# Performance work log

Measured on AMD Instinct MI355X. Metric: run time of the kernel, lower is better.

The kernel has to match this reference:

```python
import jax, jax.numpy as jnp
import numpy as np

VOCAB = 50257
EMBED = 256
UNITS = 1024   # dec_units == attention units == GRU units
ENC_D = 1024   # encoder feature dim
B = 64
T_ENC = 128


def setup_inputs() -> dict:
    key = jax.random.key(0)
    ks = jax.random.split(key, 16)
    s = lambda k, *sh: jax.random.normal(k, sh, dtype=jnp.float32) * 0.02
    gru_in = ENC_D + EMBED  # concat(context, embedding)
    return {
        "x": jax.random.randint(ks[0], (B, 1), 0, VOCAB),
        "hidden": jax.random.normal(ks[1], (B, UNITS), dtype=jnp.float32),
        "enc_output": jax.random.normal(ks[2], (B, T_ENC, ENC_D), dtype=jnp.float32),
        "emb": s(ks[3], VOCAB, EMBED),
        "W1": s(ks[4], UNITS, UNITS), "b1": jnp.zeros((UNITS,), jnp.float32),
        "W2": s(ks[5], ENC_D, UNITS), "b2": jnp.zeros((UNITS,), jnp.float32),
        "V": s(ks[6], UNITS, 1), "bV": jnp.zeros((1,), jnp.float32),
        "gru_kernel": s(ks[7], gru_in, 3 * UNITS),
        "gru_rkernel": s(ks[8], UNITS, 3 * UNITS),
        "gru_bias": jnp.zeros((2, 3 * UNITS), jnp.float32),  # reset_after=True: [input_bias, recurrent_bias]
        "fcW": s(ks[9], UNITS, VOCAB), "fcb": jnp.zeros((VOCAB,), jnp.float32),
    }


def reference(x, hidden, enc_output, emb, W1, b1, W2, b2, V, bV,
              gru_kernel, gru_rkernel, gru_bias, fcW, fcb):
    # --- Bahdanau attention ---
    q = hidden[:, None, :] @ W1 + b1                    # [B,1,U]
    k = enc_output @ W2 + b2                            # [B,T,U]
    score = jnp.tanh(q + k) @ V + bV                    # [B,T,1]
    attw = jax.nn.softmax(score, axis=1)                # [B,T,1]
    context = jnp.sum(attw * enc_output, axis=1)        # [B,ENC_D]

    # --- embed token and concat (single time step) ---
    e = emb[x[:, 0]]                                    # [B,EMBED]
    xin = jnp.concatenate([context, e], axis=-1)        # [B,ENC_D+EMBED]

    # --- single GRU step (keras default reset_after=True), initial state zeros
    # (original code calls self.gru(x) without initial_state) ---
    h0 = jnp.zeros((xin.shape[0], UNITS), xin.dtype)
    xz, xr, xh = jnp.split(xin @ gru_kernel + gru_bias[0], 3, axis=-1)
    rz, rr, rh = jnp.split(h0 @ gru_rkernel + gru_bias[1], 3, axis=-1)
    z = jax.nn.sigmoid(xz + rz)
    r = jax.nn.sigmoid(xr + rr)
    hh = jnp.tanh(xh + r * rh)
    h = z * h0 + (1.0 - z) * hh                          # [B,U]

    logits = h @ fcW + fcb                               # [B,VOCAB]
    return logits, h, attw
```

## Files before the change

### kernel.cpp

```cpp
#include <hip/hip_runtime.h>
#include <hip/hip_bf16.h>

#define UNITS 1024
#define EMBED 256
#define TENC  128
#define BATCH 64
#define VOCAB 50257
#define GRU_IN 1280
#define MROWS 8192
#define NCB   8
#define NSPLIT 8

typedef __bf16 bf16x8 __attribute__((ext_vector_type(8)));
typedef float  f32x4  __attribute__((ext_vector_type(4)));
typedef float  f32x4u __attribute__((ext_vector_type(4), aligned(4)));

__device__ __forceinline__ void gload_lds16(const void* gsrc, void* ldst) {
  __builtin_amdgcn_global_load_lds(
      (const __attribute__((address_space(1))) void*)gsrc,
      (__attribute__((address_space(3))) void*)ldst,
      16, 0, 0);
}

__global__ __launch_bounds__(256) void prep_kernel(
    const float* __restrict__ enc, const float* __restrict__ W2,
    const float* __restrict__ hidden, const float* __restrict__ W1,
    __bf16* __restrict__ encb, __bf16* __restrict__ w2t,
    float* __restrict__ qpart)
{
  __shared__ __bf16 tl[64][72];
  __shared__ __bf16 As[2][4][64][8];
  __shared__ __bf16 Bs[2][4][64][8];
  const int bid = blockIdx.x;
  const int tid = threadIdx.x;

  if (bid < 4096) {
    const size_t base = ((size_t)bid * 256 + tid) * 8;
    const f32x4 v0 = *reinterpret_cast<const f32x4*>(enc + base);
    const f32x4 v1 = *reinterpret_cast<const f32x4*>(enc + base + 4);
    bf16x8 o;
#pragma unroll
    for (int j = 0; j < 4; ++j) { o[j] = (__bf16)v0[j]; o[4 + j] = (__bf16)v1[j]; }
    *reinterpret_cast<bf16x8*>(encb + base) = o;
    return;
  }
  if (bid < 4352) {
    const int ti  = bid - 4096;
    const int kt0 = (ti >> 4) * 64, nt0 = (ti & 15) * 64;
    const int r = tid >> 2, q = (tid & 3) * 16;
    const float* wp = W2 + (size_t)(kt0 + r) * UNITS + nt0 + q;
#pragma unroll
    for (int v = 0; v < 4; ++v) {
      const f32x4 a = *reinterpret_cast<const f32x4*>(wp + v * 4);
#pragma unroll
      for (int j = 0; j < 4; ++j) tl[r][q + v * 4 + j] = (__bf16)a[j];
    }
    __syncthreads();
    const int n = tid >> 2, kq = (tid & 3) * 16;
    bf16x8 o0, o1;
#pragma unroll
    for (int j = 0; j < 8; ++j) { o0[j] = tl[kq + j][n]; o1[j] = tl[kq + 8 + j][n]; }
    __bf16* op = w2t + (size_t)(nt0 + n) * UNITS + kt0 + kq;
    *reinterpret_cast<bf16x8*>(op)     = o0;
    *reinterpret_cast<bf16x8*>(op + 8) = o1;
    return;
  }

  const int idx   = bid - 4352;
  const int col0  = (idx & 15) * 64;
  const int kbase = (idx >> 4) * 128;
  const int lane = tid & 63;
  const int wid  = tid >> 6;
  const int wm   = (wid >> 1) * 32;
  const int wn   = (wid & 1) * 32;

  f32x4 acc[2][2] = {};
  const int ar  = tid >> 2;
  const int akc = (tid & 3) * 8;
  const int bkk = tid >> 4;
  const int bn  = (tid & 15) * 4;

  f32x4 pa0[2], pa1[2], pb0[2], pb1[2];
  auto LOAD = [&](int k0, int s) {
    const float* ap = hidden + (size_t)ar * UNITS + k0 + akc;
    pa0[s] = *reinterpret_cast<const f32x4*>(ap);
    pa1[s] = *reinterpret_cast<const f32x4*>(ap + 4);
    const float* bp0 = W1 + (size_t)(k0 + bkk) * UNITS + col0 + bn;
    pb0[s] = *reinterpret_cast<const f32x4*>(bp0);
    pb1[s] = *reinterpret_cast<const f32x4*>(bp0 + (size_t)16 * UNITS);
  };
  auto STAGE = [&](int s, int bb) {
    bf16x8 v;
#pragma unroll
    for (int j = 0; j < 4; ++j) { v[j] = (__bf16)pa0[s][j]; v[4 + j] = (__bf16)pa1[s][j]; }
    *reinterpret_cast<bf16x8*>(&As[bb][tid & 3][ar][0]) = v;
#pragma unroll
    for (int j = 0; j < 4; ++j) {
      Bs[bb][bkk >> 3][bn + j][bkk & 7]               = (__bf16)pb0[s][j];
      Bs[bb][(bkk + 16) >> 3][bn + j][(bkk + 16) & 7] = (__bf16)pb1[s][j];
    }
  };
  auto COMPUTE = [&](int bb) {
    bf16x8 af[2], bfr[2];
#pragma unroll
    for (int f = 0; f < 2; ++f) {
      af[f]  = *reinterpret_cast<const bf16x8*>(&As[bb][lane >> 4][wm + f * 16 + (lane & 15)][0]);
      bfr[f] = *reinterpret_cast<const bf16x8*>(&Bs[bb][lane >> 4][wn + f * 16 + (lane & 15)][0]);
    }
#pragma unroll
    for (int fm = 0; fm < 2; ++fm)
#pragma unroll
      for (int fn = 0; fn < 2; ++fn)
        acc[fm][fn] = __builtin_amdgcn_mfma_f32_16x16x32_bf16(af[fm], bfr[fn], acc[fm][fn], 0, 0, 0);
  };

  LOAD(kbase, 0);
  LOAD(kbase + 32, 1);
  STAGE(0, 0);
  __syncthreads();
#pragma unroll 1
  for (int t = 0; t < 4; t += 2) {
    if (t + 2 < 4) LOAD(kbase + ((t + 2) << 5), 0);
    COMPUTE(0);
    STAGE(1, 1);
    __syncthreads();
    if (t + 3 < 4) LOAD(kbase + ((t + 3) << 5), 1);
    COMPUTE(1);
    if (t + 2 < 4) STAGE(0, 0);
    __syncthreads();
  }

  float* Cz = qpart + (size_t)(idx >> 4) * BATCH * UNITS;
#pragma unroll
  for (int fm = 0; fm < 2; ++fm) {
    const int rbase = wm + fm * 16 + (lane >> 4) * 4;
#pragma unroll
    for (int fn = 0; fn < 2; ++fn) {
      const int gc = col0 + wn + fn * 16 + (lane & 15);
#pragma unroll
      for (int r = 0; r < 4; ++r)
        Cz[(size_t)(rbase + r) * UNITS + gc] = acc[fm][fn][r];
    }
  }
}

__global__ __launch_bounds__(256) void gemm_splitk(
    const float* __restrict__ A, const float* __restrict__ B,
    float* __restrict__ Cpart, int M, int N, int K, int Kc)
{
  const int col0  = blockIdx.y * 64;
  const int kbase = blockIdx.z * Kc;
  const int tid  = threadIdx.x;
  const int lane = tid & 63;
  const int wid  = tid >> 6;
  const int wm   = (wid >> 1) * 32;
  const int wn   = (wid & 1) * 32;

  __shared__ __bf16 As[2][4][64][8];
  __shared__ __bf16 Bs[2][4][64][8];

  f32x4 acc[2][2] = {};

  const int ar  = tid >> 2;
  const int akc = (tid & 3) * 8;
  const int bkk = tid >> 4;
  const int bn  = (tid & 15) * 4;

  f32x4 pa0[2], pa1[2], pb0[2], pb1[2];

  auto LOAD = [&](int k0, int s) {
    const float* ap = A + (size_t)ar * K + k0 + akc;
    pa0[s] = *reinterpret_cast<const f32x4*>(ap);
    pa1[s] = *reinterpret_cast<const f32x4*>(ap + 4);
    const float* bp0 = B + (size_t)(k0 + bkk) * N + col0 + bn;
    pb0[s] = *reinterpret_cast<const f32x4*>(bp0);
    pb1[s] = *reinterpret_cast<const f32x4*>(bp0 + (size_t)16 * N);
  };
  auto STAGE = [&](int s, int bb) {
    bf16x8 v;
#pragma unroll
    for (int j = 0; j < 4; ++j) { v[j] = (__bf16)pa0[s][j]; v[4 + j] = (__bf16)pa1[s][j]; }
    *reinterpret_cast<bf16x8*>(&As[bb][tid & 3][ar][0]) = v;
#pragma unroll
    for (int j = 0; j < 4; ++j) {
      Bs[bb][bkk >> 3][bn + j][bkk & 7]               = (__bf16)pb0[s][j];
      Bs[bb][(bkk + 16) >> 3][bn + j][(bkk + 16) & 7] = (__bf16)pb1[s][j];
    }
  };
  auto COMPUTE = [&](int bb) {
    bf16x8 af[2], bfr[2];
#pragma unroll
    for (int f = 0; f < 2; ++f) {
      af[f]  = *reinterpret_cast<const bf16x8*>(&As[bb][lane >> 4][wm + f * 16 + (lane & 15)][0]);
      bfr[f] = *reinterpret_cast<const bf16x8*>(&Bs[bb][lane >> 4][wn + f * 16 + (lane & 15)][0]);
    }
#pragma unroll
    for (int fm = 0; fm < 2; ++fm)
#pragma unroll
      for (int fn = 0; fn < 2; ++fn)
        acc[fm][fn] = __builtin_amdgcn_mfma_f32_16x16x32_bf16(af[fm], bfr[fn], acc[fm][fn], 0, 0, 0);
  };

  const int nt = Kc >> 5;
  LOAD(kbase, 0);
  LOAD(kbase + 32, 1);
  STAGE(0, 0);
  __syncthreads();
  for (int t = 0; t < nt; t += 2) {
    if (t + 2 < nt) LOAD(kbase + ((t + 2) << 5), 0);
    COMPUTE(0);
    if (t + 1 < nt) STAGE(1, 1);
    __syncthreads();
    if (t + 1 < nt) {
      if (t + 3 < nt) LOAD(kbase + ((t + 3) << 5), 1);
      COMPUTE(1);
      if (t + 2 < nt) STAGE(0, 0);
      __syncthreads();
    }
  }

  float* Cz = Cpart + (size_t)blockIdx.z * M * N;
#pragma unroll
  for (int fm = 0; fm < 2; ++fm) {
    const int rbase = wm + fm * 16 + (lane >> 4) * 4;
#pragma unroll
    for (int fn = 0; fn < 2; ++fn) {
      const int gc = col0 + wn + fn * 16 + (lane & 15);
#pragma unroll
      for (int r = 0; r < 4; ++r)
        Cz[(size_t)(rbase + r) * N + gc] = acc[fm][fn][r];
    }
  }
}

__global__ __launch_bounds__(256) void gemm_fc(
    const float* __restrict__ A, const float* __restrict__ B,
    const float* __restrict__ bias, float* __restrict__ C, int N)
{
  const int col0 = blockIdx.x * 64;
  const int tid  = threadIdx.x;
  const int lane = tid & 63;
  const int wid  = tid >> 6;
  const int wm   = (wid >> 1) * 32;
  const int wn   = (wid & 1) * 32;

  __shared__ __bf16 As[2][4][64][8];
  __shared__ __bf16 Bs[2][4][64][8];

  f32x4 acc[2][2] = {};

  const int ar  = tid >> 2;
  const int akc = (tid & 3) * 8;
  const int bkk = tid >> 4;
  const int bn  = (tid & 15) * 4;
  const int gn  = col0 + bn;
  const bool okb = (gn + 3 < N);

  f32x4 pa0[2], pa1[2], pb0[2], pb1[2];

  auto LOAD = [&](int k0, int s) {
    const float* ap = A + (size_t)ar * UNITS + k0 + akc;
    pa0[s] = *reinterpret_cast<const f32x4*>(ap);
    pa1[s] = *reinterpret_cast<const f32x4*>(ap + 4);
    const float* bp0 = B + (size_t)(k0 + bkk) * N + gn;
    const float* bp1 = bp0 + (size_t)16 * N;
    if (okb) {
      pb0[s] = *reinterpret_cast<const f32x4u*>(bp0);
      pb1[s] = *reinterpret_cast<const f32x4u*>(bp1);
    } else {
      f32x4 t0 = {0,0,0,0}, t1 = {0,0,0,0};
#pragma unroll
      for (int j = 0; j < 4; ++j)
        if (gn + j < N) { t0[j] = bp0[j]; t1[j] = bp1[j]; }
      pb0[s] = t0; pb1[s] = t1;
    }
  };
  auto STAGE = [&](int s, int bb) {
    bf16x8 v;
#pragma unroll
    for (int j = 0; j < 4; ++j) { v[j] = (__bf16)pa0[s][j]; v[4 + j] = (__bf16)pa1[s][j]; }
    *reinterpret_cast<bf16x8*>(&As[bb][tid & 3][ar][0]) = v;
#pragma unroll
    for (int j = 0; j < 4; ++j) {
      Bs[bb][bkk >> 3][bn + j][bkk & 7]               = (__bf16)pb0[s][j];
      Bs[bb][(bkk + 16) >> 3][bn + j][(bkk + 16) & 7] = (__bf16)pb1[s][j];
    }
  };
  auto COMPUTE = [&](int bb) {
    bf16x8 af[2], bfr[2];
#pragma unroll
    for (int f = 0; f < 2; ++f) {
      af[f]  = *reinterpret_cast<const bf16x8*>(&As[bb][lane >> 4][wm + f * 16 + (lane & 15)][0]);
      bfr[f] = *reinterpret_cast<const bf16x8*>(&Bs[bb][lane >> 4][wn + f * 16 + (lane & 15)][0]);
    }
#pragma unroll
    for (int fm = 0; fm < 2; ++fm)
#pragma unroll
      for (int fn = 0; fn < 2; ++fn)
        acc[fm][fn] = __builtin_amdgcn_mfma_f32_16x16x32_bf16(af[fm], bfr[fn], acc[fm][fn], 0, 0, 0);
  };

  LOAD(0, 0);
  LOAD(32, 1);
  STAGE(0, 0);
  __syncthreads();
#pragma unroll 1
  for (int t = 0; t < 32; t += 2) {
    if (t + 2 < 32) LOAD((t + 2) << 5, 0);
    COMPUTE(0);
    STAGE(1, 1);
    __syncthreads();
    if (t + 3 < 32) LOAD((t + 3) << 5, 1);
    COMPUTE(1);
    if (t + 2 < 32) STAGE(0, 0);
    __syncthreads();
  }

#pragma unroll
  for (int fm = 0; fm < 2; ++fm) {
    const int rbase = wm + fm * 16 + (lane >> 4) * 4;
#pragma unroll
    for (int fn = 0; fn < 2; ++fn) {
      const int gc = col0 + wn + fn * 16 + (lane & 15);
      if (gc >= N) continue;
      const float bv = bias[gc];
#pragma unroll
      for (int r = 0; r < 4; ++r)
        __builtin_nontemporal_store(acc[fm][fn][r] + bv, &C[(size_t)(rbase + r) * N + gc]);
    }
  }
}

__global__ __launch_bounds__(256) void k_score_mfma(
    const __bf16* __restrict__ encb, const __bf16* __restrict__ w2t,
    const float* __restrict__ b1, const float* __restrict__ b2,
    const float* __restrict__ qpart, const float* __restrict__ Vw,
    float* __restrict__ partial)
{
  const int b    = blockIdx.x;
  const int row0 = b * TENC;
  const int col0 = blockIdx.y * 128;
  const int tid  = threadIdx.x;
  const int lane = tid & 63;
  const int wid  = tid >> 6;
  const int wm   = (wid >> 1) * 64;
  const int wn   = (wid & 1) * 64;

  __shared__ __bf16 As[8][128][8];
  __shared__ __bf16 Bs[8][128][8];
  __shared__ float  sred[2][128];

  f32x4 acc[4][4] = {};

  for (int t = 0; t < 16; ++t) {
    const int k0 = t * 64;
#pragma unroll
    for (int j = 0; j < 4; ++j) {
      const int i  = wid * 4 + j;
      const int c  = i >> 1, rh = (i & 1) * 64;
      gload_lds16(encb + (size_t)(row0 + rh + lane) * UNITS + k0 + c * 8, &As[c][rh][0]);
      gload_lds16(w2t  + (size_t)(col0 + rh + lane) * UNITS + k0 + c * 8, &Bs[c][rh][0]);
    }
    __syncthreads();

#pragma unroll
    for (int s = 0; s < 2; ++s) {
      bf16x8 af[4], bfr[4];
#pragma unroll
      for (int f = 0; f < 4; ++f) {
        af[f]  = *reinterpret_cast<const bf16x8*>(&As[s * 4 + (lane >> 4)][wm + f * 16 + (lane & 15)][0]);
        bfr[f] = *reinterpret_cast<const bf16x8*>(&Bs[s * 4 + (lane >> 4)][wn + f * 16 + (lane & 15)][0]);
      }
#pragma unroll
      for (int fm = 0; fm < 4; ++fm)
#pragma unroll
        for (int fn = 0; fn < 4; ++fn)
          acc[fm][fn] = __builtin_amdgcn_mfma_f32_16x16x32_bf16(af[fm], bfr[fn], acc[fm][fn], 0, 0, 0);
    }
    __syncthreads();
  }

  float rowsum[4][4] = {};
#pragma unroll
  for (int fn = 0; fn < 4; ++fn) {
    const int gc = col0 + wn + fn * 16 + (lane & 15);
    float qv = b1[gc] + b2[gc];
#pragma unroll
    for (int s = 0; s < NSPLIT; ++s)
      qv += qpart[(size_t)s * BATCH * UNITS + (size_t)b * UNITS + gc];
    const float vv = Vw[gc];
#pragma unroll
    for (int fm = 0; fm < 4; ++fm)
#pragma unroll
      for (int r = 0; r < 4; ++r)
        rowsum[fm][r] += tanhf(qv + acc[fm][fn][r]) * vv;
  }
#pragma unroll
  for (int off = 8; off; off >>= 1)
#pragma unroll
    for (int fm = 0; fm < 4; ++fm)
#pragma unroll
      for (int r = 0; r < 4; ++r)
        rowsum[fm][r] += __shfl_xor(rowsum[fm][r], off);
  if ((lane & 15) == 0) {
#pragma unroll
    for (int fm = 0; fm < 4; ++fm)
#pragma unroll
      for (int r = 0; r < 4; ++r)
        sred[wid & 1][wm + fm * 16 + (lane >> 4) * 4 + r] = rowsum[fm][r];
  }
  __syncthreads();
  if (tid < TENC)
    partial[(size_t)blockIdx.y * MROWS + row0 + tid] = sred[0][tid] + sred[1][tid];
}

__global__ __launch_bounds__(256) void ctx_kernel(
    const float* __restrict__ enc, const float* __restrict__ partial,
    const float* __restrict__ bV, const float* __restrict__ emb,
    const int* __restrict__ x, float* __restrict__ attw,
    float* __restrict__ xin)
{
  const int b   = blockIdx.x;
  const int yb  = blockIdx.y;
  const int tid = threadIdx.x;
  const int g   = tid >> 6;
  const int n   = tid & 63;
  __shared__ float scs[TENC];
  __shared__ float red[4];
  __shared__ float csum[4][64];

  if (tid < TENC) {
    float s = bV[0];
#pragma unroll
    for (int cb = 0; cb < NCB; ++cb) s += partial[(size_t)cb * MROWS + b * TENC + tid];
    float m = s;
#pragma unroll
    for (int off = 32; off; off >>= 1) m = fmaxf(m, __shfl_xor(m, off));
    if ((tid & 63) == 0) red[tid >> 6] = m;
    scs[tid] = s;
  }
  __syncthreads();
  const float mm = fmaxf(red[0], red[1]);
  if (tid < TENC) {
    const float e = expf(scs[tid] - mm);
    scs[tid] = e;
    float su = e;
#pragma unroll
    for (int off = 32; off; off >>= 1) su += __shfl_xor(su, off);
    if ((tid & 63) == 0) red[2 + (tid >> 6)] = su;
  }
  __syncthreads();
  const float inv = 1.f / (red[2] + red[3]);

  if (yb == 0 && tid < TENC) attw[(size_t)b * TENC + tid] = scs[tid] * inv;

  const int n0 = yb * 64;
  const float* ep = enc + ((size_t)b * TENC + g * 32) * UNITS + n0 + n;
  float c = 0.f;
#pragma unroll 8
  for (int i = 0; i < 32; ++i) c += scs[g * 32 + i] * ep[(size_t)i * UNITS];
  csum[g][n] = c;
  __syncthreads();
  if (tid < 64)
    xin[(size_t)b * GRU_IN + n0 + tid] =
        (csum[0][tid] + csum[1][tid] + csum[2][tid] + csum[3][tid]) * inv;
  if (yb == 0)
    xin[(size_t)b * GRU_IN + UNITS + tid] = emb[(size_t)x[b] * EMBED + tid];
}

__global__ __launch_bounds__(256) void gru_pw(
    const float* __restrict__ gpart, const float* __restrict__ gb0,
    const float* __restrict__ gb1, float* __restrict__ h)
{
  const int i = blockIdx.x * 256 + threadIdx.x;
  const int b = i >> 10, n = i & 1023;
  float xz = gb0[n], xr = gb0[1024 + n], xh = gb0[2048 + n];
#pragma unroll
  for (int s = 0; s < NSPLIT; ++s) {
    const float* g = gpart + (size_t)s * BATCH * 3072 + (size_t)b * 3072;
    xz += g[n]; xr += g[1024 + n]; xh += g[2048 + n];
  }
  const float rz = gb1[n], rr = gb1[1024 + n], rh = gb1[2048 + n];
  const float z = 1.f / (1.f + expf(-(xz + rz)));
  const float r = 1.f / (1.f + expf(-(xr + rr)));
  const float hh = tanhf(xh + r * rh);
  h[i] = (1.f - z) * hh;
}

extern "C" void kernel_launch(void* const* d_in, const int* in_sizes, int n_in,
                              void* d_out, int out_size, void* d_ws, size_t ws_size,
                              hipStream_t stream)
{
  (void)in_sizes; (void)n_in; (void)out_size; (void)ws_size;
  const int*   x      = (const int*)  d_in[0];
  const float* hidden = (const float*)d_in[1];
  const float* enc    = (const float*)d_in[2];
  const float* emb    = (const float*)d_in[3];
  const float* W1     = (const float*)d_in[4];
  const float* b1     = (const float*)d_in[5];
  const float* W2     = (const float*)d_in[6];
  const float* b2     = (const float*)d_in[7];
  const float* Vw     = (const float*)d_in[8];
  const float* bV     = (const float*)d_in[9];
  const float* gk     = (const float*)d_in[10];
  const float* gb     = (const float*)d_in[12];
  const float* fcW    = (const float*)d_in[13];
  const float* fcb    = (const float*)d_in[14];

  float* ws      = (float*)d_ws;
  float* qpart   = ws;
  float* partial = qpart + 524288;
  float* xin     = partial + 65536;
  float* gpart   = xin + 81920;
  __bf16* encb   = (__bf16*)(gpart + 1572864);
  __bf16* w2t    = encb + (size_t)MROWS * UNITS;

  float* out    = (float*)d_out;
  float* logits = out;
  float* hout   = out + (size_t)BATCH * VOCAB;
  float* attw   = hout + BATCH * UNITS;

  hipLaunchKernelGGL(prep_kernel, dim3(4096 + 256 + 128), dim3(256), 0, stream,
                     enc, W2, hidden, W1, encb, w2t, qpart);
  hipLaunchKernelGGL(k_score_mfma, dim3(64, NCB), dim3(256), 0, stream,
                     encb, w2t, b1, b2, qpart, Vw, partial);
  hipLaunchKernelGGL(ctx_kernel, dim3(64, 16), dim3(256), 0, stream,
                     enc, partial, bV, emb, x, attw, xin);
  hipLaunchKernelGGL(gemm_splitk, dim3(1, 48, NSPLIT), dim3(256), 0, stream,
                     xin, gk, gpart, 64, 3072, 1280, 160);
  hipLaunchKernelGGL(gru_pw, dim3(256), dim3(256), 0, stream,
                     gpart, gb, gb + 3072, hout);
  hipLaunchKernelGGL(gemm_fc, dim3((VOCAB + 63) / 64), dim3(256), 0, stream,
                     hout, fcW, fcb, logits, VOCAB);
}
```

Measured before the change: 143.2 us.

## Fuse context, GRU GEMM, gates and FC into one persistent kernel with grid barriers

Replaces four separate launches (context/softmax, split-K GRU GEMM, GRU pointwise, FC GEMM) with a single persistent kernel of 512 blocks that loops over work items and uses an atomic-counter grid barrier between phases. The goal is to remove kernel launch gaps and tail idle time between small dependent stages. It also manually unrolls the q-projection pipeline loop in prep_kernel. The risk is that the spin barrier relies on all 512 blocks being co-resident, which launch_bounds(256,2) is meant to make likely. The FC GEMM, the largest stage, now runs on only 512 blocks that loop over about 786 column tiles, so load balance may be worse than with the earlier one-block-per-tile launch.

```diff
diff --git a/kernel.cpp b/kernel.cpp
--- a/kernel.cpp
+++ b/kernel.cpp
@@ -10,6 +10,7 @@
 #define MROWS 8192
 #define NCB   8
 #define NSPLIT 8
+#define TBLK  512
 
 typedef __bf16 bf16x8 __attribute__((ext_vector_type(8)));
 typedef float  f32x4  __attribute__((ext_vector_type(4)));
@@ -26,13 +27,16 @@
     const float* __restrict__ enc, const float* __restrict__ W2,
     const float* __restrict__ hidden, const float* __restrict__ W1,
     __bf16* __restrict__ encb, __bf16* __restrict__ w2t,
-    float* __restrict__ qpart)
+    float* __restrict__ qpart, unsigned* __restrict__ syncf)
 {
   __shared__ __bf16 tl[64][72];
   __shared__ __bf16 As[2][4][64][8];
   __shared__ __bf16 Bs[2][4][64][8];
   const int bid = blockIdx.x;
   const int tid = threadIdx.x;
+
+  if (bid == 0 && tid == 0)
+    __hip_atomic_store(syncf, 0u, __ATOMIC_RELAXED, __HIP_MEMORY_SCOPE_AGENT);
 
   if (bid < 4096) {
     const size_t base = ((size_t)bid * 256 + tid) * 8;
@@ -114,21 +118,15 @@
         acc[fm][fn] = __builtin_amdgcn_mfma_f32_16x16x32_bf16(af[fm], bfr[fn], acc[fm][fn], 0, 0, 0);
   };
 
-  LOAD(kbase, 0);
-  LOAD(kbase + 32, 1);
-  STAGE(0, 0);
+  LOAD(kbase, 0); LOAD(kbase + 32, 1); STAGE(0, 0);
   __syncthreads();
-#pragma unroll 1
-  for (int t = 0; t < 4; t += 2) {
-    if (t + 2 < 4) LOAD(kbase + ((t + 2) << 5), 0);
-    COMPUTE(0);
-    STAGE(1, 1);
-    __syncthreads();
-    if (t + 3 < 4) LOAD(kbase + ((t + 3) << 5), 1);
-    COMPUTE(1);
-    if (t + 2 < 4) STAGE(0, 0);
-    __syncthreads();
-  }
+  LOAD(kbase + 64, 0); COMPUTE(0); STAGE(1, 1);
+  __syncthreads();
+  LOAD(kbase + 96, 1); COMPUTE(1); STAGE(0, 0);
+  __syncthreads();
+  COMPUTE(0); STAGE(1, 1);
+  __syncthreads();
+  COMPUTE(1);
 
   float* Cz = qpart + (size_t)(idx >> 4) * BATCH * UNITS;
 #pragma unroll
@@ -140,193 +138,6 @@
 #pragma unroll
       for (int r = 0; r < 4; ++r)
         Cz[(size_t)(rbase + r) * UNITS + gc] = acc[fm][fn][r];
-    }
-  }
-}
-
-__global__ __launch_bounds__(256) void gemm_splitk(
-    const float* __restrict__ A, const float* __restrict__ B,
-    float* __restrict__ Cpart, int M, int N, int K, int Kc)
-{
-  const int col0  = blockIdx.y * 64;
-  const int kbase = blockIdx.z * Kc;
-  const int tid  = threadIdx.x;
-  const int lane = tid & 63;
-  const int wid  = tid >> 6;
-  const int wm   = (wid >> 1) * 32;
-  const int wn   = (wid & 1) * 32;
-
-  __shared__ __bf16 As[2][4][64][8];
-  __shared__ __bf16 Bs[2][4][64][8];
-
-  f32x4 acc[2][2] = {};
-
-  const int ar  = tid >> 2;
-  const int akc = (tid & 3) * 8;
-  const int bkk = tid >> 4;
-  const int bn  = (tid & 15) * 4;
-
-  f32x4 pa0[2], pa1[2], pb0[2], pb1[2];
-
-  auto LOAD = [&](int k0, int s) {
-    const float* ap = A + (size_t)ar * K + k0 + akc;
-    pa0[s] = *reinterpret_cast<const f32x4*>(ap);
-    pa1[s] = *reinterpret_cast<const f32x4*>(ap + 4);
-    const float* bp0 = B + (size_t)(k0 + bkk) * N + col0 + bn;
-    pb0[s] = *reinterpret_cast<const f32x4*>(bp0);
-    pb1[s] = *reinterpret_cast<const f32x4*>(bp0 + (size_t)16 * N);
-  };
-  auto STAGE = [&](int s, int bb) {
-    bf16x8 v;
-#pragma unroll
-    for (int j = 0; j < 4; ++j) { v[j] = (__bf16)pa0[s][j]; v[4 + j] = (__bf16)pa1[s][j]; }
-    *reinterpret_cast<bf16x8*>(&As[bb][tid & 3][ar][0]) = v;
-#pragma unroll
-    for (int j = 0; j < 4; ++j) {
-      Bs[bb][bkk >> 3][bn + j][bkk & 7]               = (__bf16)pb0[s][j];
-      Bs[bb][(bkk + 16) >> 3][bn + j][(bkk + 16) & 7] = (__bf16)pb1[s][j];
-    }
-  };
-  auto COMPUTE = [&](int bb) {
-    bf16x8 af[2], bfr[2];
-#pragma unroll
-    for (int f = 0; f < 2; ++f) {
-      af[f]  = *reinterpret_cast<const bf16x8*>(&As[bb][lane >> 4][wm + f * 16 + (lane & 15)][0]);
-      bfr[f] = *reinterpret_cast<const bf16x8*>(&Bs[bb][lane >> 4][wn + f * 16 + (lane & 15)][0]);
-    }
-#pragma unroll
-    for (int fm = 0; fm < 2; ++fm)
-#pragma unroll
-      for (int fn = 0; fn < 2; ++fn)
-        acc[fm][fn] = __builtin_amdgcn_mfma_f32_16x16x32_bf16(af[fm], bfr[fn], acc[fm][fn], 0, 0, 0);
-  };
-
-  const int nt = Kc >> 5;
-  LOAD(kbase, 0);
-  LOAD(kbase + 32, 1);
-  STAGE(0, 0);
-  __syncthreads();
-  for (int t = 0; t < nt; t += 2) {
-    if (t + 2 < nt) LOAD(kbase + ((t + 2) << 5), 0);
-    COMPUTE(0);
-    if (t + 1 < nt) STAGE(1, 1);
-    __syncthreads();
-    if (t + 1 < nt) {
-      if (t + 3 < nt) LOAD(kbase + ((t + 3) << 5), 1);
-      COMPUTE(1);
-      if (t + 2 < nt) STAGE(0, 0);
-      __syncthreads();
-    }
-  }
-
-  float* Cz = Cpart + (size_t)blockIdx.z * M * N;
-#pragma unroll
-  for (int fm = 0; fm < 2; ++fm) {
-    const int rbase = wm + fm * 16 + (lane >> 4) * 4;
-#pragma unroll
-    for (int fn = 0; fn < 2; ++fn) {
-      const int gc = col0 + wn + fn * 16 + (lane & 15);
-#pragma unroll
-      for (int r = 0; r < 4; ++r)
-        Cz[(size_t)(rbase + r) * N + gc] = acc[fm][fn][r];
-    }
-  }
-}
-
-__global__ __launch_bounds__(256) void gemm_fc(
-    const float* __restrict__ A, const float* __restrict__ B,
-    const float* __restrict__ bias, float* __restrict__ C, int N)
-{
-  const int col0 = blockIdx.x * 64;
-  const int tid  = threadIdx.x;
-  const int lane = tid & 63;
-  const int wid  = tid >> 6;
-  const int wm   = (wid >> 1) * 32;
-  const int wn   = (wid & 1) * 32;
-
-  __shared__ __bf16 As[2][4][64][8];
-  __shared__ __bf16 Bs[2][4][64][8];
-
-  f32x4 acc[2][2] = {};
-
-  const int ar  = tid >> 2;
-  const int akc = (tid & 3) * 8;
-  const int bkk = tid >> 4;
-  const int bn  = (tid & 15) * 4;
-  const int gn  = col0 + bn;
-  const bool okb = (gn + 3 < N);
-
-  f32x4 pa0[2], pa1[2], pb0[2], pb1[2];
-
-  auto LOAD = [&](int k0, int s) {
-    const float* ap = A + (size_t)ar * UNITS + k0 + akc;
-    pa0[s] = *reinterpret_cast<const f32x4*>(ap);
-    pa1[s] = *reinterpret_cast<const f32x4*>(ap + 4);
-    const float* bp0 = B + (size_t)(k0 + bkk) * N + gn;
-    const float* bp1 = bp0 + (size_t)16 * N;
-    if (okb) {
-      pb0[s] = *reinterpret_cast<const f32x4u*>(bp0);
-      pb1[s] = *reinterpret_cast<const f32x4u*>(bp1);
-    } else {
-      f32x4 t0 = {0,0,0,0}, t1 = {0,0,0,0};
-#pragma unroll
-      for (int j = 0; j < 4; ++j)
-        if (gn + j < N) { t0[j] = bp0[j]; t1[j] = bp1[j]; }
-      pb0[s] = t0; pb1[s] = t1;
-    }
-  };
-  auto STAGE = [&](int s, int bb) {
-    bf16x8 v;
-#pragma unroll
-    for (int j = 0; j < 4; ++j) { v[j] = (__bf16)pa0[s][j]; v[4 + j] = (__bf16)pa1[s][j]; }
-    *reinterpret_cast<bf16x8*>(&As[bb][tid & 3][ar][0]) = v;
-#pragma unroll
-    for (int j = 0; j < 4; ++j) {
-      Bs[bb][bkk >> 3][bn + j][bkk & 7]               = (__bf16)pb0[s][j];
-      Bs[bb][(bkk + 16) >> 3][bn + j][(bkk + 16) & 7] = (__bf16)pb1[s][j];
-    }
-  };
-  auto COMPUTE = [&](int bb) {
-    bf16x8 af[2], bfr[2];
-#pragma unroll
-    for (int f = 0; f < 2; ++f) {
-      af[f]  = *reinterpret_cast<const bf16x8*>(&As[bb][lane >> 4][wm + f * 16 + (lane & 15)][0]);
-      bfr[f] = *reinterpret_cast<const bf16x8*>(&Bs[bb][lane >> 4][wn + f * 16 + (lane & 15)][0]);
-    }
-#pragma unroll
-    for (int fm = 0; fm < 2; ++fm)
-#pragma unroll
-      for (int fn = 0; fn < 2; ++fn)
-        acc[fm][fn] = __builtin_amdgcn_mfma_f32_16x16x32_bf16(af[fm], bfr[fn], acc[fm][fn], 0, 0, 0);
-  };
-
-  LOAD(0, 0);
-  LOAD(32, 1);
-  STAGE(0, 0);
-  __syncthreads();
-#pragma unroll 1
-  for (int t = 0; t < 32; t += 2) {
-    if (t + 2 < 32) LOAD((t + 2) << 5, 0);
-    COMPUTE(0);
-    STAGE(1, 1);
-    __syncthreads();
-    if (t + 3 < 32) LOAD((t + 3) << 5, 1);
-    COMPUTE(1);
-    if (t + 2 < 32) STAGE(0, 0);
-    __syncthreads();
-  }
-
-#pragma unroll
-  for (int fm = 0; fm < 2; ++fm) {
-    const int rbase = wm + fm * 16 + (lane >> 4) * 4;
-#pragma unroll
-    for (int fn = 0; fn < 2; ++fn) {
-      const int gc = col0 + wn + fn * 16 + (lane & 15);
-      if (gc >= N) continue;
-      const float bv = bias[gc];
-#pragma unroll
-      for (int r = 0; r < 4; ++r)
-        __builtin_nontemporal_store(acc[fm][fn][r] + bv, &C[(size_t)(rbase + r) * N + gc]);
     }
   }
 }
@@ -362,7 +173,6 @@
       gload_lds16(w2t  + (size_t)(col0 + rh + lane) * UNITS + k0 + c * 8, &Bs[c][rh][0]);
     }
     __syncthreads();
-
 #pragma unroll
     for (int s = 0; s < 2; ++s) {
       bf16x8 af[4], bfr[4];
@@ -414,77 +224,253 @@
     partial[(size_t)blockIdx.y * MROWS + row0 + tid] = sred[0][tid] + sred[1][tid];
 }
 
-__global__ __launch_bounds__(256) void ctx_kernel(
+union TailSMem {
+  struct { __bf16 A[2][4][64][8]; __bf16 B[2][4][64][8]; } gm;
+  struct { float scs[TENC]; float red[4]; float csum[4][64]; } cx;
+};
+
+__global__ __launch_bounds__(256, 2) void tail_kernel(
     const float* __restrict__ enc, const float* __restrict__ partial,
     const float* __restrict__ bV, const float* __restrict__ emb,
-    const int* __restrict__ x, float* __restrict__ attw,
-    float* __restrict__ xin)
+    const int* __restrict__ x, const float* __restrict__ gk,
+    const float* __restrict__ gb, const float* __restrict__ fcW,
+    const float* __restrict__ fcb, float* __restrict__ attw,
+    float* __restrict__ xin, float* __restrict__ gpart,
+    float* __restrict__ hout, float* __restrict__ logits,
+    unsigned* __restrict__ syncf)
 {
-  const int b   = blockIdx.x;
-  const int yb  = blockIdx.y;
-  const int tid = threadIdx.x;
-  const int g   = tid >> 6;
-  const int n   = tid & 63;
-  __shared__ float scs[TENC];
-  __shared__ float red[4];
-  __shared__ float csum[4][64];
-
-  if (tid < TENC) {
-    float s = bV[0];
-#pragma unroll
-    for (int cb = 0; cb < NCB; ++cb) s += partial[(size_t)cb * MROWS + b * TENC + tid];
-    float m = s;
-#pragma unroll
-    for (int off = 32; off; off >>= 1) m = fmaxf(m, __shfl_xor(m, off));
-    if ((tid & 63) == 0) red[tid >> 6] = m;
-    scs[tid] = s;
-  }
-  __syncthreads();
-  const float mm = fmaxf(red[0], red[1]);
-  if (tid < TENC) {
-    const float e = expf(scs[tid] - mm);
-    scs[tid] = e;
-    float su = e;
-#pragma unroll
-    for (int off = 32; off; off >>= 1) su += __shfl_xor(su, off);
-    if ((tid & 63) == 0) red[2 + (tid >> 6)] = su;
-  }
-  __syncthreads();
-  const float inv = 1.f / (red[2] + red[3]);
-
-  if (yb == 0 && tid < TENC) attw[(size_t)b * TENC + tid] = scs[tid] * inv;
-
-  const int n0 = yb * 64;
-  const float* ep = enc + ((size_t)b * TENC + g * 32) * UNITS + n0 + n;
-  float c = 0.f;
+  __shared__ TailSMem sm;
+  const int bid  = blockIdx.x;
+  const int tid  = threadIdx.x;
+  const int lane = tid & 63;
+  const int wid  = tid >> 6;
+
+  auto GRID_SYNC = [&](unsigned tgt) {
+    __syncthreads();
+    if (tid == 0) {
+      __threadfence();
+      __hip_atomic_fetch_add(syncf, 1u, __ATOMIC_ACQ_REL, __HIP_MEMORY_SCOPE_AGENT);
+      while (__hip_atomic_load(syncf, __ATOMIC_ACQUIRE, __HIP_MEMORY_SCOPE_AGENT) < tgt)
+        __builtin_amdgcn_s_sleep(2);
+    }
+    __syncthreads();
+  };
+
+  for (int item = bid; item < 1024; item += TBLK) {
+    __syncthreads();
+    const int b  = item & 63;
+    const int yb = item >> 6;
+    const int gq = tid >> 6;
+    const int n  = tid & 63;
+    if (tid < TENC) {
+      float s = bV[0];
+#pragma unroll
+      for (int cb = 0; cb < NCB; ++cb) s += partial[(size_t)cb * MROWS + b * TENC + tid];
+      float m = s;
+#pragma unroll
+      for (int off = 32; off; off >>= 1) m = fmaxf(m, __shfl_xor(m, off));
+      if ((tid & 63) == 0) sm.cx.red[tid >> 6] = m;
+      sm.cx.scs[tid] = s;
+    }
+    __syncthreads();
+    const float mm = fmaxf(sm.cx.red[0], sm.cx.red[1]);
+    if (tid < TENC) {
+      const float e = expf(sm.cx.scs[tid] - mm);
+      sm.cx.scs[tid] = e;
+      float su = e;
+#pragma unroll
+      for (int off = 32; off; off >>= 1) su += __shfl_xor(su, off);
+      if ((tid & 63) == 0) sm.cx.red[2 + (tid >> 6)] = su;
+    }
+    __syncthreads();
+    const float inv = 1.f / (sm.cx.red[2] + sm.cx.red[3]);
+    if (yb == 0 && tid < TENC) attw[(size_t)b * TENC + tid] = sm.cx.scs[tid] * inv;
+
+    const int n0 = yb * 64;
+    const float* ep = enc + ((size_t)b * TENC + gq * 32) * UNITS + n0 + n;
+    float c = 0.f;
 #pragma unroll 8
-  for (int i = 0; i < 32; ++i) c += scs[g * 32 + i] * ep[(size_t)i * UNITS];
-  csum[g][n] = c;
-  __syncthreads();
-  if (tid < 64)
-    xin[(size_t)b * GRU_IN + n0 + tid] =
-        (csum[0][tid] + csum[1][tid] + csum[2][tid] + csum[3][tid]) * inv;
-  if (yb == 0)
-    xin[(size_t)b * GRU_IN + UNITS + tid] = emb[(size_t)x[b] * EMBED + tid];
-}
-
-__global__ __launch_bounds__(256) void gru_pw(
-    const float* __restrict__ gpart, const float* __restrict__ gb0,
-    const float* __restrict__ gb1, float* __restrict__ h)
-{
-  const int i = blockIdx.x * 256 + threadIdx.x;
-  const int b = i >> 10, n = i & 1023;
-  float xz = gb0[n], xr = gb0[1024 + n], xh = gb0[2048 + n];
-#pragma unroll
-  for (int s = 0; s < NSPLIT; ++s) {
-    const float* g = gpart + (size_t)s * BATCH * 3072 + (size_t)b * 3072;
-    xz += g[n]; xr += g[1024 + n]; xh += g[2048 + n];
-  }
-  const float rz = gb1[n], rr = gb1[1024 + n], rh = gb1[2048 + n];
-  const float z = 1.f / (1.f + expf(-(xz + rz)));
-  const float r = 1.f / (1.f + expf(-(xr + rr)));
-  const float hh = tanhf(xh + r * rh);
-  h[i] = (1.f - z) * hh;
+    for (int i = 0; i < 32; ++i) c += sm.cx.scs[gq * 32 + i] * ep[(size_t)i * UNITS];
+    sm.cx.csum[gq][n] = c;
+    __syncthreads();
+    if (tid < 64)
+      xin[(size_t)b * GRU_IN + n0 + tid] =
+          (sm.cx.csum[0][tid] + sm.cx.csum[1][tid] + sm.cx.csum[2][tid] + sm.cx.csum[3][tid]) * inv;
+    if (yb == 0)
+      xin[(size_t)b * GRU_IN + UNITS + tid] = emb[(size_t)x[b] * EMBED + tid];
+  }
+  GRID_SYNC(TBLK);
+
+  for (int item = bid; item < 384; item += TBLK) {
+    __syncthreads();
+    const int y = item % 48, z = item / 48;
+    const int col0 = y * 64, kbase = z * 160;
+    const int wm = (wid >> 1) * 32, wn = (wid & 1) * 32;
+    f32x4 acc[2][2] = {};
+    const int ar  = tid >> 2;
+    const int akc = (tid & 3) * 8;
+    const int bkk = tid >> 4;
+    const int bn  = (tid & 15) * 4;
+    f32x4 pa0[2], pa1[2], pb0[2], pb1[2];
+    auto LOAD = [&](int k0, int s) {
+      const float* ap = xin + (size_t)ar * GRU_IN + k0 + akc;
+      pa0[s] = *reinterpret_cast<const f32x4*>(ap);
+      pa1[s] = *reinterpret_cast<const f32x4*>(ap + 4);
+      const float* bp0 = gk + (size_t)(k0 + bkk) * 3072 + col0 + bn;
+      pb0[s] = *reinterpret_cast<const f32x4*>(bp0);
+      pb1[s] = *reinterpret_cast<const f32x4*>(bp0 + (size_t)16 * 3072);
+    };
+    auto STAGE = [&](int s, int bb) {
+      bf16x8 v;
+#pragma unroll
+      for (int j = 0; j < 4; ++j) { v[j] = (__bf16)pa0[s][j]; v[4 + j] = (__bf16)pa1[s][j]; }
+      *reinterpret_cast<bf16x8*>(&sm.gm.A[bb][tid & 3][ar][0]) = v;
+#pragma unroll
+      for (int j = 0; j < 4; ++j) {
+        sm.gm.B[bb][bkk >> 3][bn + j][bkk & 7]               = (__bf16)pb0[s][j];
+        sm.gm.B[bb][(bkk + 16) >> 3][bn + j][(bkk + 16) & 7] = (__bf16)pb1[s][j];
+      }
+    };
+    auto COMPUTE = [&](int bb) {
+      bf16x8 af[2], bfr[2];
+#pragma unroll
+      for (int f = 0; f < 2; ++f) {
+        af[f]  = *reinterpret_cast<const bf16x8*>(&sm.gm.A[bb][lane >> 4][wm + f * 16 + (lane & 15)][0]);
+        bfr[f] = *reinterpret_cast<const bf16x8*>(&sm.gm.B[bb][lane >> 4][wn + f * 16 + (lane & 15)][0]);
+      }
+#pragma unroll
+      for (int fm = 0; fm < 2; ++fm)
+#pragma unroll
+        for (int fn = 0; fn < 2; ++fn)
+          acc[fm][fn] = __builtin_amdgcn_mfma_f32_16x16x32_bf16(af[fm], bfr[fn], acc[fm][fn], 0, 0, 0);
+    };
+    LOAD(kbase, 0); LOAD(kbase + 32, 1); STAGE(0, 0);
+    __syncthreads();
+    for (int t = 0; t < 5; t += 2) {
+      if (t + 2 < 5) LOAD(kbase + ((t + 2) << 5), 0);
+      COMPUTE(0);
+      if (t + 1 < 5) STAGE(1, 1);
+      __syncthreads();
+      if (t + 1 < 5) {
+        if (t + 3 < 5) LOAD(kbase + ((t + 3) << 5), 1);
+        COMPUTE(1);
+        if (t + 2 < 5) STAGE(0, 0);
+        __syncthreads();
+      }
+    }
+    float* Cz = gpart + (size_t)z * BATCH * 3072;
+#pragma unroll
+    for (int fm = 0; fm < 2; ++fm) {
+      const int rbase = wm + fm * 16 + (lane >> 4) * 4;
+#pragma unroll
+      for (int fn = 0; fn < 2; ++fn) {
+        const int gc = col0 + wn + fn * 16 + (lane & 15);
+#pragma unroll
+        for (int r = 0; r < 4; ++r)
+          Cz[(size_t)(rbase + r) * 3072 + gc] = acc[fm][fn][r];
+      }
+    }
+  }
+  GRID_SYNC(2 * TBLK);
+
+  for (int item = bid; item < 256; item += TBLK) {
+    const int i = item * 256 + tid;
+    const int b = i >> 10, n = i & 1023;
+    float xz = gb[n], xr = gb[1024 + n], xh = gb[2048 + n];
+#pragma unroll
+    for (int s = 0; s < NSPLIT; ++s) {
+      const float* g = gpart + (size_t)s * BATCH * 3072 + (size_t)b * 3072;
+      xz += g[n]; xr += g[1024 + n]; xh += g[2048 + n];
+    }
+    const float* gb1p = gb + 3072;
+    const float rz = gb1p[n], rr = gb1p[1024 + n], rh = gb1p[2048 + n];
+    const float z = 1.f / (1.f + expf(-(xz + rz)));
+    const float r = 1.f / (1.f + expf(-(xr + rr)));
+    const float hh = tanhf(xh + r * rh);
+    hout[i] = (1.f - z) * hh;
+  }
+  GRID_SYNC(3 * TBLK);
+
+  for (int item = bid; item < (VOCAB + 63) / 64; item += TBLK) {
+    __syncthreads();
+    const int col0 = item * 64;
+    const int wm = (wid >> 1) * 32, wn = (wid & 1) * 32;
+    f32x4 acc[2][2] = {};
+    const int ar  = tid >> 2;
+    const int akc = (tid & 3) * 8;
+    const int bkk = tid >> 4;
+    const int bn  = (tid & 15) * 4;
+    const int gn  = col0 + bn;
+    const bool okb = (gn + 3 < VOCAB);
+    f32x4 pa0[2], pa1[2], pb0[2], pb1[2];
+    auto LOAD = [&](int k0, int s) {
+      const float* ap = hout + (size_t)ar * UNITS + k0 + akc;
+      pa0[s] = *reinterpret_cast<const f32x4*>(ap);
+      pa1[s] = *reinterpret_cast<const f32x4*>(ap + 4);
+      const float* bp0 = fcW + (size_t)(k0 + bkk) * VOCAB + gn;
+      const float* bp1 = bp0 + (size_t)16 * VOCAB;
+      if (okb) {
+        pb0[s] = *reinterpret_cast<const f32x4u*>(bp0);
+        pb1[s] = *reinterpret_cast<const f32x4u*>(bp1);
+      } else {
+        f32x4 t0 = {0,0,0,0}, t1 = {0,0,0,0};
+#pragma unroll
+        for (int j = 0; j < 4; ++j)
+          if (gn + j < VOCAB) { t0[j] = bp0[j]; t1[j] = bp1[j]; }
+        pb0[s] = t0; pb1[s] = t1;
+      }
+    };
+    auto STAGE = [&](int s, int bb) {
+      bf16x8 v;
+#pragma unroll
+      for (int j = 0; j < 4; ++j) { v[j] = (__bf16)pa0[s][j]; v[4 + j] = (__bf16)pa1[s][j]; }
+      *reinterpret_cast<bf16x8*>(&sm.gm.A[bb][tid & 3][ar][0]) = v;
+#pragma unroll
+      for (int j = 0; j < 4; ++j) {
+        sm.gm.B[bb][bkk >> 3][bn + j][bkk & 7]               = (__bf16)pb0[s][j];
+        sm.gm.B[bb][(bkk + 16) >> 3][bn + j][(bkk + 16) & 7] = (__bf16)pb1[s][j];
+      }
+    };
+    auto COMPUTE = [&](int bb) {
+      bf16x8 af[2], bfr[2];
+#pragma unroll
+      for (int f = 0; f < 2; ++f) {
+        af[f]  = *reinterpret_cast<const bf16x8*>(&sm.gm.A[bb][lane >> 4][wm + f * 16 + (lane & 15)][0]);
+        bfr[f] = *reinterpret_cast<const bf16x8*>(&sm.gm.B[bb][lane >> 4][wn + f * 16 + (lane & 15)][0]);
+      }
+#pragma unroll
+      for (int fm = 0; fm < 2; ++fm)
+#pragma unroll
+        for (int fn = 0; fn < 2; ++fn)
+          acc[fm][fn] = __builtin_amdgcn_mfma_f32_16x16x32_bf16(af[fm], bfr[fn], acc[fm][fn], 0, 0, 0);
+    };
+    LOAD(0, 0); LOAD(32, 1); STAGE(0, 0);
+    __syncthreads();
+#pragma unroll 1
+    for (int t = 0; t < 32; t += 2) {
+      if (t + 2 < 32) LOAD((t + 2) << 5, 0);
+      COMPUTE(0);
+      STAGE(1, 1);
+      __syncthreads();
+      if (t + 3 < 32) LOAD((t + 3) << 5, 1);
+      COMPUTE(1);
+      if (t + 2 < 32) STAGE(0, 0);
+      __syncthreads();
+    }
+#pragma unroll
+    for (int fm = 0; fm < 2; ++fm) {
+      const int rbase = wm + fm * 16 + (lane >> 4) * 4;
+#pragma unroll
+      for (int fn = 0; fn < 2; ++fn) {
+        const int gc = col0 + wn + fn * 16 + (lane & 15);
+        if (gc >= VOCAB) continue;
+        const float bv = fcb[gc];
+#pragma unroll
+        for (int r = 0; r < 4; ++r)
+          __builtin_nontemporal_store(acc[fm][fn][r] + bv, &logits[(size_t)(rbase + r) * VOCAB + gc]);
+      }
+    }
+  }
 }
 
 extern "C" void kernel_launch(void* const* d_in, const int* in_sizes, int n_in,
@@ -507,13 +493,14 @@
   const float* fcW    = (const float*)d_in[13];
   const float* fcb    = (const float*)d_in[14];
 
-  float* ws      = (float*)d_ws;
-  float* qpart   = ws;
-  float* partial = qpart + 524288;
-  float* xin     = partial + 65536;
-  float* gpart   = xin + 81920;
-  __bf16* encb   = (__bf16*)(gpart + 1572864);
-  __bf16* w2t    = encb + (size_t)MROWS * UNITS;
+  float* ws       = (float*)d_ws;
+  float* qpart    = ws;
+  float* partial  = qpart + 524288;
+  float* xin      = partial + 65536;
+  float* gpart    = xin + 81920;
+  __bf16* encb    = (__bf16*)(gpart + 1572864);
+  __bf16* w2t     = encb + (size_t)MROWS * UNITS;
+  unsigned* syncf = (unsigned*)(w2t + (size_t)UNITS * UNITS);
 
   float* out    = (float*)d_out;
   float* logits = out;
@@ -521,15 +508,10 @@
   float* attw   = hout + BATCH * UNITS;
 
   hipLaunchKernelGGL(prep_kernel, dim3(4096 + 256 + 128), dim3(256), 0, stream,
-                     enc, W2, hidden, W1, encb, w2t, qpart);
+                     enc, W2, hidden, W1, encb, w2t, qpart, syncf);
   hipLaunchKernelGGL(k_score_mfma, dim3(64, NCB), dim3(256), 0, stream,
                      encb, w2t, b1, b2, qpart, Vw, partial);
-  hipLaunchKernelGGL(ctx_kernel, dim3(64, 16), dim3(256), 0, stream,
-                     enc, partial, bV, emb, x, attw, xin);
-  hipLaunchKernelGGL(gemm_splitk, dim3(1, 48, NSPLIT), dim3(256), 0, stream,
-                     xin, gk, gpart, 64, 3072, 1280, 160);
-  hipLaunchKernelGGL(gru_pw, dim3(256), dim3(256), 0, stream,
-                     gpart, gb, gb + 3072, hout);
-  hipLaunchKernelGGL(gemm_fc, dim3((VOCAB + 63) / 64), dim3(256), 0, stream,
-                     hout, fcW, fcb, logits, VOCAB);
+  hipLaunchKernelGGL(tail_kernel, dim3(TBLK), dim3(256), 0, stream,
+                     enc, partial, bV, emb, x, gk, gb, fcW, fcb,
+                     attw, xin, gpart, hout, logits, syncf);
 }
```

Result: slower. 317.3 us, median of 2 (+121.6%).
